# Performance work log

Hardware: AMD Instinct MI355X
Metric: run time of the kernel (lower is better)

Reference implementation:

```python
import jax, jax.numpy as jnp
import numpy as np

B, H, W = 8, 56, 56
DIM = 1792      # 256 + 512 + 1024 concatenated WRN50-2 feature channels
C_OUT = 1792    # dim // gamma_d with gamma_d = 1
M = 3136        # memory bank entries = scale**2 // gamma_c (gamma_c = 1)
K = 3           # num_nearest_neighbors


def setup_inputs() -> dict:
    key = jax.random.key(0)
    ks = jax.random.split(key, 6)
    f1 = jax.random.normal(ks[0], (B, 256, 56, 56), jnp.float32)
    f2 = jax.random.normal(ks[1], (B, 512, 28, 28), jnp.float32)
    f3 = jax.random.normal(ks[2], (B, 1024, 14, 14), jnp.float32)
    conv_w = jax.random.normal(ks[3], (C_OUT, DIM + 2), jnp.float32) / np.float32(np.sqrt(DIM + 2))
    conv_b = jax.random.normal(ks[4], (C_OUT,), jnp.float32) * 0.01
    memory_bank = jax.random.normal(ks[5], (C_OUT, M), jnp.float32)
    return {"f1": f1, "f2": f2, "f3": f3, "conv_w": conv_w, "conv_b": conv_b,
            "memory_bank": memory_bank}


def _avg_pool3(x):
    # F.avg_pool2d(x, 3, 1, 1), count_include_pad=True (torch default)
    s = jax.lax.reduce_window(x, 0.0, jax.lax.add, (1, 1, 3, 3), (1, 1, 1, 1),
                              ((0, 0), (0, 0), (1, 1), (1, 1)))
    return s / 9.0


def _descriptor(f1, f2, f3, conv_w, conv_b):
    o1 = _avg_pool3(f1)                                                    # [B,256,56,56]
    o2 = jax.image.resize(_avg_pool3(f2), (B, 512, H, W), method="bilinear")
    o3 = jax.image.resize(_avg_pool3(f3), (B, 1024, H, W), method="bilinear")
    sample = jnp.concatenate([o1, o2, o3], axis=1)                         # [B,DIM,H,W]
    # CoordConv: append x and y coordinate channels in [-1, 1]
    xx = jnp.tile(jnp.linspace(-1.0, 1.0, W, dtype=sample.dtype)[None, :], (H, 1))
    yy = jnp.tile(jnp.linspace(-1.0, 1.0, H, dtype=sample.dtype)[:, None], (1, W))
    coords = jnp.broadcast_to(jnp.stack([xx, yy])[None], (B, 2, H, W))
    inp = jnp.concatenate([sample, coords], axis=1)                        # [B,DIM+2,H,W]
    # 1x1 conv == per-pixel GEMM
    return jnp.einsum("bchw,oc->bohw", inp, conv_w) + conv_b[None, :, None, None]


def reference(f1, f2, f3, conv_w, conv_b, memory_bank):
    phi = _descriptor(f1, f2, f3, conv_w, conv_b)          # [B,C,H,W]
    feats = phi.reshape(B, C_OUT, H * W).transpose(0, 2, 1)  # [B,HW,C]
    # squared-distance expansion vs memory bank [C,M]
    f_sq = jnp.sum(feats * feats, axis=2, keepdims=True)     # [B,HW,1]
    c_sq = jnp.sum(memory_bank * memory_bank, axis=0, keepdims=True)  # [1,M]
    dist = f_sq + c_sq - 2.0 * jnp.einsum("bnc,cm->bnm", feats, memory_bank)  # [B,HW,M]
    dist = jnp.sqrt(dist)
    neg_top, _ = jax.lax.top_k(-dist, K)   # smallest K, ascending after negation
    d_k = -neg_top                         # [B,HW,K] sorted ascending
    w = jax.nn.softmax(-d_k, axis=-1)      # softmin
    score = w[:, :, 0] * d_k[:, :, 0]      # [B,HW]
    return score.reshape(B, 1, H, W)
```

## Files before the change

### kernel.cpp

```cpp
#include <hip/hip_runtime.h>
#include <hip/hip_bf16.h>
#include <math.h>

#define HH 56
#define WW 56
#define HWv 3136
#define NROWS 25088
#define DIMK 1792
#define KP   1920
#define CIN 1794
#define COUT 1792
#define MM 3136
#define MROWS 3328
#define JT2 13
#define JT1 7
#define NT 98

typedef __bf16 bf16_t;
typedef __bf16 bf16x8 __attribute__((ext_vector_type(8)));
typedef float f32x4 __attribute__((ext_vector_type(4)));

__device__ __forceinline__ void merge3(float& d0, float& d1, float& d2,
                                       float e0, float e1, float e2) {
    bool t0 = d0 <= e0;
    float c0 = t0 ? d0 : e0;
    float x0 = t0 ? d1 : d0, x1 = t0 ? d2 : d1;
    float y0 = t0 ? e0 : e1, y1 = t0 ? e1 : e2;
    bool t1 = x0 <= y0;
    float c1 = t1 ? x0 : y0;
    float c2 = t1 ? fminf(x1, y0) : fminf(x0, y1);
    d0 = c0; d1 = c1; d2 = c2;
}

__device__ __forceinline__ int xcd_swz(int wg, int nwg) {
    int x = wg & 7, idx = wg >> 3;
    int q = nwg >> 3, r = nwg & 7;
    return (x < r ? x * (q + 1) : r * (q + 1) + (x - r) * q) + idx;
}

__device__ __forceinline__ void block_bar() {
    asm volatile("" ::: "memory");
    __builtin_amdgcn_s_barrier();
    asm volatile("" ::: "memory");
}


__global__ __launch_bounds__(256) void k_convw(const float* __restrict__ cw, bf16_t* __restrict__ wb) {
    int idx = blockIdx.x * 256 + threadIdx.x;
    if (idx >= COUT * DIMK) return;
    int o = idx / DIMK, c = idx - o * DIMK;
    wb[(size_t)o * KP + c] = (bf16_t)cw[(size_t)o * CIN + c];
}

__global__ __launch_bounds__(256) void k_bankT(const float* __restrict__ bank, bf16_t* __restrict__ bt) {
    __shared__ float tile[64][65];
    int mt = blockIdx.x * 64;
    int ct = blockIdx.y * 64;
    int l = threadIdx.x & 63;
    int q = threadIdx.x >> 6;
    if (mt < MM) {
        #pragma unroll
        for (int r = 0; r < 16; ++r) {
            int cl = q * 16 + r;
            tile[cl][l] = bank[(size_t)(ct + cl) * MM + mt + l];
        }
        __syncthreads();
        #pragma unroll
        for (int r = 0; r < 16; ++r) {
            int ml = q * 16 + r;
            bt[(size_t)(mt + ml) * KP + ct + l] = (bf16_t)tile[l][ml];
        }
    } else {
        #pragma unroll
        for (int r = 0; r < 16; ++r) {
            int ml = q * 16 + r;
            bt[(size_t)(mt + ml) * KP + ct + l] = (bf16_t)0.f;
        }
    }
}

__global__ __launch_bounds__(256) void k_rowsq(const bf16_t* __restrict__ rows, float* __restrict__ sq) {
    int n = blockIdx.x * 4 + (threadIdx.x >> 6);
    int lane = threadIdx.x & 63;
    const bf16x8* row = (const bf16x8*)(rows + (size_t)n * KP);
    float s = 0.f;
    #pragma unroll
    for (int t = 0; t < 4; ++t) {
        int idx = t * 64 + lane;
        if (idx < 224) {
            bf16x8 v = row[idx];
            #pragma unroll
            for (int j = 0; j < 8; ++j) { float f = (float)v[j]; s += f * f; }
        }
    }
    #pragma unroll
    for (int off = 32; off; off >>= 1) s += __shfl_xor(s, off, 64);
    if (lane == 0) sq[n] = s;
}

__global__ __launch_bounds__(256) void k_pool_s(const float* __restrict__ in, float* __restrict__ out,
                                                int S, int total) {
    int idx = blockIdx.x * 256 + threadIdx.x;
    if (idx >= total) return;
    int x = idx % S; int y = (idx / S) % S; int bc = idx / (S * S);
    const float* base = in + (size_t)bc * S * S;
    float s = 0.f;
    for (int dy = -1; dy <= 1; ++dy) {
        int yy = y + dy; if ((unsigned)yy >= (unsigned)S) continue;
        for (int dx = -1; dx <= 1; ++dx) {
            int xx = x + dx; if ((unsigned)xx >= (unsigned)S) continue;
            s += base[yy * S + xx];
        }
    }
    out[idx] = s * (1.f / 9.f);
}

__global__ __launch_bounds__(256) void k_resize_p(const float* __restrict__ src, bf16_t* __restrict__ dst,
                                                  int S, int total, float scale, float shift) {
    int idx = blockIdx.x * 256 + threadIdx.x;
    if (idx >= total) return;
    int w = idx % WW; int h = (idx / WW) % HH; int bc = idx / HWv;
    float sy = scale * h + shift;
    float sx = scale * w + shift;
    float y0f = floorf(sy), x0f = floorf(sx);
    int y0 = (int)y0f, x0 = (int)x0f;
    float fy = sy - y0f, fx = sx - x0f;
    int iy0 = y0 < 0 ? 0 : (y0 > S - 1 ? S - 1 : y0);
    int iy1 = (y0 + 1) < 0 ? 0 : ((y0 + 1) > S - 1 ? S - 1 : y0 + 1);
    int ix0 = x0 < 0 ? 0 : (x0 > S - 1 ? S - 1 : x0);
    int ix1 = (x0 + 1) < 0 ? 0 : ((x0 + 1) > S - 1 ? S - 1 : x0 + 1);
    const float* base = src + (size_t)bc * S * S;
    float v00 = base[iy0 * S + ix0], v01 = base[iy0 * S + ix1];
    float v10 = base[iy1 * S + ix0], v11 = base[iy1 * S + ix1];
    float v = (1.f - fy) * ((1.f - fx) * v00 + fx * v01) + fy * ((1.f - fx) * v10 + fx * v11);
    dst[idx] = (bf16_t)v;
}

template <typename T>
__global__ __launch_bounds__(256) void k_transp(const T* __restrict__ src, bf16_t* __restrict__ inp,
                                                int Csrc, int coff) {
    __shared__ float tile[64][65];
    int hw0 = blockIdx.x * 64;
    int c0 = blockIdx.y * 64;
    int b = blockIdx.z;
    int l = threadIdx.x & 63;
    int q = threadIdx.x >> 6;
    #pragma unroll
    for (int r = 0; r < 16; ++r) {
        int c = q * 16 + r;
        tile[c][l] = (float)src[(size_t)(b * Csrc + c0 + c) * HWv + hw0 + l];
    }
    __syncthreads();
    #pragma unroll
    for (int r = 0; r < 16; ++r) {
        int ml = q * 16 + r;
        inp[(size_t)(b * HWv + hw0 + ml) * KP + coff + c0 + l] = (bf16_t)tile[l][ml];
    }
}


__device__ __forceinline__ void gemm256(const bf16_t* __restrict__ A, const bf16_t* __restrict__ Bm,
                                        int n0, int j0, f32x4 (&acc)[8][4], bf16_t* lds) {
    const int tid = threadIdx.x;
    const int lane = tid & 63;
    const int wid = tid >> 6;
    const int wr = wid >> 2;
    const int wc = wid & 3;
    const int lr = lane & 15;
    const int lg = lane >> 4;

    bf16_t* sA = lds;
    bf16_t* sB = lds + 32768;

    #pragma unroll
    for (int i = 0; i < 8; ++i)
        #pragma unroll
        for (int j = 0; j < 4; ++j) acc[i][j] = (f32x4){0.f, 0.f, 0.f, 0.f};

    auto stage = [&](bf16_t* dst, const bf16_t* src, int row0, int kc) {
        #pragma unroll
        for (int r = 0; r < 2; ++r) {
            int g = r * 512 + tid;
            int rp = g >> 2;
            int gc = g & 3;
            int gcs = gc ^ ((rp >> 1) & 3);
            __builtin_amdgcn_global_load_lds(
                (__attribute__((address_space(1))) void*)(src + (size_t)(row0 + rp) * KP + kc + gcs * 8),
                (__attribute__((address_space(3))) void*)(dst + g * 8), 16, 0, 0);
        }
    };

#define PHASE(BUF, MH, KH, STAGE_CODE, TAIL_CODE)                                          \
    {                                                                                      \
        bf16_t* au = sA + (BUF) * 16384 + (KH) * 8192;                                     \
        bf16_t* bu = sB + (BUF) * 16384 + (KH) * 8192;                                     \
        bf16x8 aF[4], bF[4];                                                               \
        _Pragma("unroll")                                                                  \
        for (int q = 0; q < 4; ++q) {                                                      \
            int ra = wr * 128 + (MH) * 64 + q * 16 + lr;                                   \
            aF[q] = *(const bf16x8*)(au + ra * 32 + ((lg ^ ((ra >> 1) & 3)) * 8));         \
            int rb = wc * 64 + q * 16 + lr;                                                \
            bF[q] = *(const bf16x8*)(bu + rb * 32 + ((lg ^ ((rb >> 1) & 3)) * 8));         \
        }                                                                                  \
        STAGE_CODE;                                                                        \
        block_bar();                                                                       \
        __builtin_amdgcn_s_setprio(1);                                                     \
        _Pragma("unroll")                                                                  \
        for (int q = 0; q < 4; ++q)                                                        \
            _Pragma("unroll")                                                              \
            for (int fn = 0; fn < 4; ++fn)                                                 \
                acc[(MH) * 4 + q][fn] = __builtin_amdgcn_mfma_f32_16x16x32_bf16(           \
                    aF[q], bF[fn], acc[(MH) * 4 + q][fn], 0, 0, 0);                        \
        __builtin_amdgcn_s_setprio(0);                                                     \
        TAIL_CODE;                                                                         \
        block_bar();                                                                       \
    }

    stage(sA + 0,             A,  n0, 0);
    stage(sB + 0,             Bm, j0, 0);
    stage(sA + 8192,          A,  n0, 32);
    stage(sB + 8192,          Bm, j0, 32);
    stage(sA + 16384,         A,  n0, 64);
    stage(sB + 16384,         Bm, j0, 64);
    asm volatile("s_waitcnt vmcnt(4)" ::: "memory");
    block_bar();

    for (int i = 0; i < 14; ++i) {
        int k1 = (2 * i + 1) * 64, k2 = (2 * i + 2) * 64, k3 = (2 * i + 3) * 64;
        PHASE(0, 0, 0, { stage(sA + 16384 + 8192, A,  n0, k1 + 32); }, {});
        PHASE(0, 1, 0, { stage(sB + 16384 + 8192, Bm, j0, k1 + 32); }, {});
        PHASE(0, 0, 1, { stage(sA + 0,            A,  n0, k2); }, {});
        PHASE(0, 1, 1, { stage(sB + 0,            Bm, j0, k2); },
              { asm volatile("s_waitcnt vmcnt(4)" ::: "memory"); });
        PHASE(1, 0, 0, { stage(sA + 8192,         A,  n0, k2 + 32); }, {});
        PHASE(1, 1, 0, { stage(sB + 8192,         Bm, j0, k2 + 32); }, {});
        PHASE(1, 0, 1, { stage(sA + 16384,        A,  n0, k3); }, {});
        PHASE(1, 1, 1, { stage(sB + 16384,        Bm, j0, k3); },
              { asm volatile("s_waitcnt vmcnt(4)" ::: "memory"); });
    }
    asm volatile("s_waitcnt vmcnt(0)" ::: "memory");
    block_bar();
#undef PHASE
}

__global__ __launch_bounds__(512) void k_gemm1(const bf16_t* __restrict__ inp, const bf16_t* __restrict__ wb,
                                               const float* __restrict__ cw, const float* __restrict__ cb,
                                               bf16_t* __restrict__ feats) {
    __shared__ __align__(16) bf16_t lds[65536];
    int wg = xcd_swz(blockIdx.x, NT * JT1);
    int n0 = (wg / JT1) * 256, j0 = (wg % JT1) * 256;
    f32x4 acc[8][4];
    gemm256(inp, wb, n0, j0, acc, lds);

    const int lane = threadIdx.x & 63, wid = threadIdx.x >> 6;
    const int wr = wid >> 2, wc = wid & 3, lr = lane & 15, lg = lane >> 4;
    float w1[4], w2[4], bb[4];
    int oc[4];
    #pragma unroll
    for (int fn = 0; fn < 4; ++fn) {
        int o = j0 + wc * 64 + fn * 16 + lr;
        oc[fn] = o;
        bb[fn] = cb[o];
        w1[fn] = cw[(size_t)o * CIN + DIMK];
        w2[fn] = cw[(size_t)o * CIN + DIMK + 1];
    }
    #pragma unroll
    for (int mh = 0; mh < 2; ++mh) {
        #pragma unroll
        for (int q = 0; q < 4; ++q) {
            #pragma unroll
            for (int v = 0; v < 4; ++v) {
                int n = n0 + wr * 128 + mh * 64 + q * 16 + lg * 4 + v;
                int hw = n % HWv;
                int h = hw / WW, w = hw - h * WW;
                float xx = (2.f / 55.f) * w - 1.f;
                float yy = (2.f / 55.f) * h - 1.f;
                #pragma unroll
                for (int fn = 0; fn < 4; ++fn) {
                    float phi = acc[mh * 4 + q][fn][v] + bb[fn] + xx * w1[fn] + yy * w2[fn];
                    feats[(size_t)n * KP + oc[fn]] = (bf16_t)phi;
                }
            }
        }
    }
}

__global__ __launch_bounds__(512) void k_gemm2(const bf16_t* __restrict__ feats, const bf16_t* __restrict__ bt,
                                               const float* __restrict__ csq, float* __restrict__ partial) {
    __shared__ __align__(16) bf16_t lds[65536];
    int wg = xcd_swz(blockIdx.x, NT * JT2);
    int nt = wg / JT2, jt = wg % JT2;
    int n0 = nt * 256, j0 = jt * 256;
    f32x4 acc[8][4];
    gemm256(feats, bt, n0, j0, acc, lds);

    const int tid = threadIdx.x;
    const int lane = tid & 63, wid = tid >> 6;
    const int wr = wid >> 2, wc = wid & 3, lr = lane & 15, lg = lane >> 4;

    float csqv[4];
    bool mval[4];
    #pragma unroll
    for (int fn = 0; fn < 4; ++fn) {
        int m = j0 + wc * 64 + fn * 16 + lr;
        mval[fn] = (m < MM);
        csqv[fn] = mval[fn] ? csq[m] : 0.f;
    }

    float* lf  = (float*)lds;
    float* lf2 = lf + 128 * 64 * 3;
    const int gidx = wc * 16 + lr;
    const float BIG = 3.0e38f;

    for (int pass = 0; pass < 2; ++pass) {
        if (wr == pass) {
            #pragma unroll
            for (int mh = 0; mh < 2; ++mh) {
                #pragma unroll
                for (int q = 0; q < 4; ++q) {
                    #pragma unroll
                    for (int v = 0; v < 4; ++v) {
                        float a0 = mval[0] ? csqv[0] - 2.f * acc[mh * 4 + q][0][v] : BIG;
                        float a1 = mval[1] ? csqv[1] - 2.f * acc[mh * 4 + q][1][v] : BIG;
                        float a2 = mval[2] ? csqv[2] - 2.f * acc[mh * 4 + q][2][v] : BIG;
                        float a3 = mval[3] ? csqv[3] - 2.f * acc[mh * 4 + q][3][v] : BIG;
                        float t;
                        if (a0 > a1) { t = a0; a0 = a1; a1 = t; }
                        if (a2 > a3) { t = a2; a2 = a3; a3 = t; }
                        if (a0 > a2) { t = a0; a0 = a2; a2 = t; }
                        if (a1 > a3) { t = a1; a1 = a3; a3 = t; }
                        if (a1 > a2) { t = a1; a1 = a2; a2 = t; }
                        int rl = mh * 64 + q * 16 + lg * 4 + v;
                        int bix = (rl * 64 + gidx) * 3;
                        lf[bix] = a0; lf[bix + 1] = a1; lf[bix + 2] = a2;
                    }
                }
            }
        }
        __syncthreads();
        {
            int row = tid >> 2, seg = tid & 3;
            int base = (row * 64 + seg * 16) * 3;
            float d0 = lf[base], d1 = lf[base + 1], d2 = lf[base + 2];
            #pragma unroll
            for (int j2 = 1; j2 < 16; ++j2)
                merge3(d0, d1, d2, lf[base + j2 * 3], lf[base + j2 * 3 + 1], lf[base + j2 * 3 + 2]);
            int o2 = (row * 4 + seg) * 3;
            lf2[o2] = d0; lf2[o2 + 1] = d1; lf2[o2 + 2] = d2;
        }
        __syncthreads();
        if (tid < 128) {
            int base = tid * 12;
            float d0 = lf2[base], d1 = lf2[base + 1], d2 = lf2[base + 2];
            #pragma unroll
            for (int sg = 1; sg < 4; ++sg)
                merge3(d0, d1, d2, lf2[base + sg * 3], lf2[base + sg * 3 + 1], lf2[base + sg * 3 + 2]);
            size_t grow = (size_t)(n0 + pass * 128 + tid);
            float* pp = partial + grow * (JT2 * 3) + jt * 3;
            pp[0] = d0; pp[1] = d1; pp[2] = d2;
        }
        __syncthreads();
    }
}

__global__ __launch_bounds__(256) void k_score(const float* __restrict__ partial, const float* __restrict__ fsq,
                                               float* __restrict__ out) {
    int row = blockIdx.x * 256 + threadIdx.x;
    if (row >= NROWS) return;
    const float* p = partial + (size_t)row * (JT2 * 3);
    float d0 = p[0], d1 = p[1], d2 = p[2];
    #pragma unroll
    for (int jt = 1; jt < JT2; ++jt)
        merge3(d0, d1, d2, p[jt * 3], p[jt * 3 + 1], p[jt * 3 + 2]);
    float fs = fsq[row];
    d0 = sqrtf(fmaxf(fs + d0, 0.f));
    d1 = sqrtf(fmaxf(fs + d1, 0.f));
    d2 = sqrtf(fmaxf(fs + d2, 0.f));
    float e1 = expf(d0 - d1), e2 = expf(d0 - d2);
    out[row] = d0 / (1.f + e1 + e2);
}


extern "C" void kernel_launch(void* const* d_in, const int* in_sizes, int n_in,
                              void* d_out, int out_size, void* d_ws, size_t ws_size,
                              hipStream_t stream) {
    const float* f1   = (const float*)d_in[0];
    const float* f2   = (const float*)d_in[1];
    const float* f3   = (const float*)d_in[2];
    const float* cw   = (const float*)d_in[3];
    const float* cb   = (const float*)d_in[4];
    const float* bank = (const float*)d_in[5];
    float* out = (float*)d_out;
    char* ws = (char*)d_ws;

    size_t off = 0;
    auto alloc = [&](size_t bytes) { size_t o = off; off = (off + bytes + 255) & ~(size_t)255; return o; };
    bf16_t* wb      = (bf16_t*)(ws + alloc((size_t)COUT * KP * 2));
    bf16_t* bt      = (bf16_t*)(ws + alloc((size_t)MROWS * KP * 2));
    float*  fsq     = (float*)(ws + alloc((size_t)NROWS * 4));
    float*  csq     = (float*)(ws + alloc((size_t)MM * 4));
    float*  partial = (float*)(ws + alloc((size_t)NROWS * JT2 * 3 * 4));
    bf16_t* inp     = (bf16_t*)(ws + alloc((size_t)NROWS * KP * 2));
    bf16_t* feats   = (bf16_t*)(ws + alloc((size_t)NROWS * KP * 2));

    char* fb = (char*)feats;
    float*  p1  = (float*)fb;
    float*  p2s = (float*)(fb + 25690112);
    bf16_t* r2b = (bf16_t*)(fb + 25690112 + 12845056);
    float*  p3s = (float*)fb;
    bf16_t* r3b = (bf16_t*)(fb + 6422528);

    k_convw<<<dim3((COUT * DIMK + 255) / 256), dim3(256), 0, stream>>>(cw, wb);
    k_bankT<<<dim3(MROWS / 64, DIMK / 64), dim3(256), 0, stream>>>(bank, bt);
    k_rowsq<<<dim3(MM / 4), dim3(256), 0, stream>>>(bt, csq);

    k_pool_s<<<dim3((8 * 256 * HWv + 255) / 256), dim3(256), 0, stream>>>(f1, p1, 56, 8 * 256 * HWv);
    k_pool_s<<<dim3((8 * 512 * 784 + 255) / 256), dim3(256), 0, stream>>>(f2, p2s, 28, 8 * 512 * 784);
    k_resize_p<<<dim3((8 * 512 * HWv + 255) / 256), dim3(256), 0, stream>>>(p2s, r2b, 28, 8 * 512 * HWv, 0.5f, -0.25f);
    k_transp<float><<<dim3(HWv / 64, 256 / 64, 8), dim3(256), 0, stream>>>(p1, inp, 256, 0);
    k_transp<bf16_t><<<dim3(HWv / 64, 512 / 64, 8), dim3(256), 0, stream>>>(r2b, inp, 512, 256);
    k_pool_s<<<dim3((8 * 1024 * 196 + 255) / 256), dim3(256), 0, stream>>>(f3, p3s, 14, 8 * 1024 * 196);
    k_resize_p<<<dim3((8 * 1024 * HWv + 255) / 256), dim3(256), 0, stream>>>(p3s, r3b, 14, 8 * 1024 * HWv, 0.25f, -0.375f);
    k_transp<bf16_t><<<dim3(HWv / 64, 1024 / 64, 8), dim3(256), 0, stream>>>(r3b, inp, 1024, 768);

    k_gemm1<<<dim3(NT * JT1), dim3(512), 0, stream>>>(inp, wb, cw, cb, feats);
    k_rowsq<<<dim3(NROWS / 4), dim3(256), 0, stream>>>(feats, fsq);
    k_gemm2<<<dim3(NT * JT2), dim3(512), 0, stream>>>(feats, bt, csq, partial);
    k_score<<<dim3((NROWS + 255) / 256), dim3(256), 0, stream>>>(partial, fsq, out);
}
```

Baseline: 753.1 us.

## Restructure GEMM mainloop into ring-buffered K-slices and use shuffle top-3 reduction

Replaces the double-buffered phase macro in the shared 256x256 GEMM with a rolling ring of 5 A slots and 4 B slots (K=32 each). Each iteration loads all 8x4 fragments, issues the next stage, and runs 32 MFMAs per barrier. Addresses and swizzle offsets are precomputed, and the LDS swizzle is reworked to pair rows. The gemm2 epilogue now does its top-3 merge with cross-lane shuffles instead of two-pass LDS staging, which cuts LDS traffic and barriers. The cost is more LDS per block (144KB) and higher register pressure from holding all fragments at once.

```diff
diff --git a/kernel.cpp b/kernel.cpp
--- a/kernel.cpp
+++ b/kernel.cpp
@@ -15,6 +15,7 @@
 #define JT2 13
 #define JT1 7
 #define NT 98
+#define NPH 56
 
 typedef __bf16 bf16_t;
 typedef __bf16 bf16x8 __attribute__((ext_vector_type(8)));
@@ -170,83 +171,107 @@
     const int lg = lane >> 4;
 
     bf16_t* sA = lds;
-    bf16_t* sB = lds + 32768;
-
-    #pragma unroll
-    for (int i = 0; i < 8; ++i)
-        #pragma unroll
-        for (int j = 0; j < 4; ++j) acc[i][j] = (f32x4){0.f, 0.f, 0.f, 0.f};
-
-    auto stage = [&](bf16_t* dst, const bf16_t* src, int row0, int kc) {
-        #pragma unroll
-        for (int r = 0; r < 2; ++r) {
-            int g = r * 512 + tid;
-            int rp = g >> 2;
-            int gc = g & 3;
-            int gcs = gc ^ ((rp >> 1) & 3);
+    bf16_t* sB = lds + 40960;
+
+    #pragma unroll
+    for (int m = 0; m < 8; ++m)
+        #pragma unroll
+        for (int n = 0; n < 4; ++n) acc[m][n] = (f32x4){0.f, 0.f, 0.f, 0.f};
+
+    size_t srcA[2], srcB[2];
+    int ldso[2];
+    #pragma unroll
+    for (int r = 0; r < 2; ++r) {
+        int g = r * 512 + tid;
+        int r2 = g >> 3, S = g & 7;
+        int G = S ^ (r2 & 7);
+        int row = 2 * r2 + (G >> 2);
+        int kgr = G & 3;
+        srcA[r] = (size_t)(n0 + row) * KP + kgr * 8;
+        srcB[r] = (size_t)(j0 + row) * KP + kgr * 8;
+        ldso[r] = g * 8;
+    }
+    auto stageA = [&](int slotOff, int kc) {
+        #pragma unroll
+        for (int r = 0; r < 2; ++r)
             __builtin_amdgcn_global_load_lds(
-                (__attribute__((address_space(1))) void*)(src + (size_t)(row0 + rp) * KP + kc + gcs * 8),
-                (__attribute__((address_space(3))) void*)(dst + g * 8), 16, 0, 0);
-        }
+                (__attribute__((address_space(1))) void*)(A + srcA[r] + kc),
+                (__attribute__((address_space(3))) void*)(sA + slotOff + ldso[r]), 16, 0, 0);
     };
-
-#define PHASE(BUF, MH, KH, STAGE_CODE, TAIL_CODE)                                          \
-    {                                                                                      \
-        bf16_t* au = sA + (BUF) * 16384 + (KH) * 8192;                                     \
-        bf16_t* bu = sB + (BUF) * 16384 + (KH) * 8192;                                     \
-        bf16x8 aF[4], bF[4];                                                               \
-        _Pragma("unroll")                                                                  \
-        for (int q = 0; q < 4; ++q) {                                                      \
-            int ra = wr * 128 + (MH) * 64 + q * 16 + lr;                                   \
-            aF[q] = *(const bf16x8*)(au + ra * 32 + ((lg ^ ((ra >> 1) & 3)) * 8));         \
-            int rb = wc * 64 + q * 16 + lr;                                                \
-            bF[q] = *(const bf16x8*)(bu + rb * 32 + ((lg ^ ((rb >> 1) & 3)) * 8));         \
-        }                                                                                  \
-        STAGE_CODE;                                                                        \
-        block_bar();                                                                       \
-        __builtin_amdgcn_s_setprio(1);                                                     \
-        _Pragma("unroll")                                                                  \
-        for (int q = 0; q < 4; ++q)                                                        \
-            _Pragma("unroll")                                                              \
-            for (int fn = 0; fn < 4; ++fn)                                                 \
-                acc[(MH) * 4 + q][fn] = __builtin_amdgcn_mfma_f32_16x16x32_bf16(           \
-                    aF[q], bF[fn], acc[(MH) * 4 + q][fn], 0, 0, 0);                        \
-        __builtin_amdgcn_s_setprio(0);                                                     \
-        TAIL_CODE;                                                                         \
-        block_bar();                                                                       \
-    }
-
-    stage(sA + 0,             A,  n0, 0);
-    stage(sB + 0,             Bm, j0, 0);
-    stage(sA + 8192,          A,  n0, 32);
-    stage(sB + 8192,          Bm, j0, 32);
-    stage(sA + 16384,         A,  n0, 64);
-    stage(sB + 16384,         Bm, j0, 64);
-    asm volatile("s_waitcnt vmcnt(4)" ::: "memory");
+    auto stageB = [&](int slotOff, int kc) {
+        #pragma unroll
+        for (int r = 0; r < 2; ++r)
+            __builtin_amdgcn_global_load_lds(
+                (__attribute__((address_space(1))) void*)(Bm + srcB[r] + kc),
+                (__attribute__((address_space(3))) void*)(sB + slotOff + ldso[r]), 16, 0, 0);
+    };
+
+    int offA[8], offB[4];
+    #pragma unroll
+    for (int m = 0; m < 8; ++m) {
+        int rowU = wr * 128 + m * 16 + lr;
+        int r2 = rowU >> 1, par = rowU & 1;
+        int G = par * 4 + lg;
+        offA[m] = r2 * 64 + (G ^ (r2 & 7)) * 8;
+    }
+    #pragma unroll
+    for (int n = 0; n < 4; ++n) {
+        int colU = wc * 64 + n * 16 + lr;
+        int r2 = colU >> 1, par = colU & 1;
+        int G = par * 4 + lg;
+        offB[n] = r2 * 64 + (G ^ (r2 & 7)) * 8;
+    }
+
+    stageA(0 * 8192, 0 * 32);
+    stageA(1 * 8192, 1 * 32);
+    stageB(0 * 8192, 0 * 32);
+    stageA(2 * 8192, 2 * 32);
+    stageB(1 * 8192, 1 * 32);
+    stageA(3 * 8192, 3 * 32);
+    stageB(2 * 8192, 2 * 32);
+    asm volatile("s_waitcnt vmcnt(8)" ::: "memory");
     block_bar();
 
-    for (int i = 0; i < 14; ++i) {
-        int k1 = (2 * i + 1) * 64, k2 = (2 * i + 2) * 64, k3 = (2 * i + 3) * 64;
-        PHASE(0, 0, 0, { stage(sA + 16384 + 8192, A,  n0, k1 + 32); }, {});
-        PHASE(0, 1, 0, { stage(sB + 16384 + 8192, Bm, j0, k1 + 32); }, {});
-        PHASE(0, 0, 1, { stage(sA + 0,            A,  n0, k2); }, {});
-        PHASE(0, 1, 1, { stage(sB + 0,            Bm, j0, k2); },
-              { asm volatile("s_waitcnt vmcnt(4)" ::: "memory"); });
-        PHASE(1, 0, 0, { stage(sA + 8192,         A,  n0, k2 + 32); }, {});
-        PHASE(1, 1, 0, { stage(sB + 8192,         Bm, j0, k2 + 32); }, {});
-        PHASE(1, 0, 1, { stage(sA + 16384,        A,  n0, k3); }, {});
-        PHASE(1, 1, 1, { stage(sB + 16384,        Bm, j0, k3); },
-              { asm volatile("s_waitcnt vmcnt(4)" ::: "memory"); });
+    int roA = 0, roB = 0;
+    int kcA = 4 * 32, kcB = 3 * 32;
+
+    for (int p = 0; p < NPH; ++p) {
+        bf16x8 aF[8], bF[4];
+        #pragma unroll
+        for (int m = 0; m < 8; ++m)
+            aF[m] = *(const bf16x8*)(sA + roA + offA[m]);
+        #pragma unroll
+        for (int n = 0; n < 4; ++n)
+            bF[n] = *(const bf16x8*)(sB + roB + offB[n]);
+
+        int stA = roA - 8192; if (stA < 0) stA = 4 * 8192;
+        int stB = roB - 8192; if (stB < 0) stB = 3 * 8192;
+        stageA(stA, kcA);
+        stageB(stB, kcB);
+        kcA += 32; kcB += 32;
+
+        __builtin_amdgcn_s_setprio(1);
+        #pragma unroll
+        for (int m = 0; m < 8; ++m)
+            #pragma unroll
+            for (int n = 0; n < 4; ++n)
+                acc[m][n] = __builtin_amdgcn_mfma_f32_16x16x32_bf16(
+                    aF[m], bF[n], acc[m][n], 0, 0, 0);
+        __builtin_amdgcn_s_setprio(0);
+
+        roA += 8192; if (roA == 5 * 8192) roA = 0;
+        roB += 8192; if (roB == 4 * 8192) roB = 0;
+        asm volatile("s_waitcnt vmcnt(8)" ::: "memory");
+        block_bar();
     }
     asm volatile("s_waitcnt vmcnt(0)" ::: "memory");
-    block_bar();
-#undef PHASE
-}
+}
+
 
 __global__ __launch_bounds__(512) void k_gemm1(const bf16_t* __restrict__ inp, const bf16_t* __restrict__ wb,
                                                const float* __restrict__ cw, const float* __restrict__ cb,
                                                bf16_t* __restrict__ feats) {
-    __shared__ __align__(16) bf16_t lds[65536];
+    __shared__ __align__(16) bf16_t lds[73728];
     int wg = xcd_swz(blockIdx.x, NT * JT1);
     int n0 = (wg / JT1) * 256, j0 = (wg % JT1) * 256;
     f32x4 acc[8][4];
@@ -257,29 +282,26 @@
     float w1[4], w2[4], bb[4];
     int oc[4];
     #pragma unroll
-    for (int fn = 0; fn < 4; ++fn) {
-        int o = j0 + wc * 64 + fn * 16 + lr;
-        oc[fn] = o;
-        bb[fn] = cb[o];
-        w1[fn] = cw[(size_t)o * CIN + DIMK];
-        w2[fn] = cw[(size_t)o * CIN + DIMK + 1];
-    }
-    #pragma unroll
-    for (int mh = 0; mh < 2; ++mh) {
-        #pragma unroll
-        for (int q = 0; q < 4; ++q) {
+    for (int n = 0; n < 4; ++n) {
+        int o = j0 + wc * 64 + n * 16 + lr;
+        oc[n] = o;
+        bb[n] = cb[o];
+        w1[n] = cw[(size_t)o * CIN + DIMK];
+        w2[n] = cw[(size_t)o * CIN + DIMK + 1];
+    }
+    #pragma unroll
+    for (int m = 0; m < 8; ++m) {
+        #pragma unroll
+        for (int v = 0; v < 4; ++v) {
+            int nrow = n0 + wr * 128 + m * 16 + lg * 4 + v;
+            int hw = nrow % HWv;
+            int h = hw / WW, w = hw - h * WW;
+            float xx = (2.f / 55.f) * w - 1.f;
+            float yy = (2.f / 55.f) * h - 1.f;
             #pragma unroll
-            for (int v = 0; v < 4; ++v) {
-                int n = n0 + wr * 128 + mh * 64 + q * 16 + lg * 4 + v;
-                int hw = n % HWv;
-                int h = hw / WW, w = hw - h * WW;
-                float xx = (2.f / 55.f) * w - 1.f;
-                float yy = (2.f / 55.f) * h - 1.f;
-                #pragma unroll
-                for (int fn = 0; fn < 4; ++fn) {
-                    float phi = acc[mh * 4 + q][fn][v] + bb[fn] + xx * w1[fn] + yy * w2[fn];
-                    feats[(size_t)n * KP + oc[fn]] = (bf16_t)phi;
-                }
+            for (int n = 0; n < 4; ++n) {
+                float phi = acc[m][n][v] + bb[n] + xx * w1[n] + yy * w2[n];
+                feats[(size_t)nrow * KP + oc[n]] = (bf16_t)phi;
             }
         }
     }
@@ -287,79 +309,69 @@
 
 __global__ __launch_bounds__(512) void k_gemm2(const bf16_t* __restrict__ feats, const bf16_t* __restrict__ bt,
                                                const float* __restrict__ csq, float* __restrict__ partial) {
-    __shared__ __align__(16) bf16_t lds[65536];
+    __shared__ __align__(16) bf16_t lds[73728];
     int wg = xcd_swz(blockIdx.x, NT * JT2);
     int nt = wg / JT2, jt = wg % JT2;
     int n0 = nt * 256, j0 = jt * 256;
     f32x4 acc[8][4];
     gemm256(feats, bt, n0, j0, acc, lds);
 
+    block_bar();
+
     const int tid = threadIdx.x;
     const int lane = tid & 63, wid = tid >> 6;
     const int wr = wid >> 2, wc = wid & 3, lr = lane & 15, lg = lane >> 4;
+    const float BIG = 3.0e38f;
 
     float csqv[4];
     bool mval[4];
     #pragma unroll
-    for (int fn = 0; fn < 4; ++fn) {
-        int m = j0 + wc * 64 + fn * 16 + lr;
-        mval[fn] = (m < MM);
-        csqv[fn] = mval[fn] ? csq[m] : 0.f;
-    }
-
-    float* lf  = (float*)lds;
-    float* lf2 = lf + 128 * 64 * 3;
-    const int gidx = wc * 16 + lr;
-    const float BIG = 3.0e38f;
-
-    for (int pass = 0; pass < 2; ++pass) {
-        if (wr == pass) {
+    for (int n = 0; n < 4; ++n) {
+        int m = j0 + wc * 64 + n * 16 + lr;
+        mval[n] = (m < MM);
+        csqv[n] = mval[n] ? csq[m] : 0.f;
+    }
+
+    float* lf = (float*)lds;
+
+    #pragma unroll
+    for (int m = 0; m < 8; ++m) {
+        #pragma unroll
+        for (int v = 0; v < 4; ++v) {
+            float a0 = mval[0] ? csqv[0] - 2.f * acc[m][0][v] : BIG;
+            float a1 = mval[1] ? csqv[1] - 2.f * acc[m][1][v] : BIG;
+            float a2 = mval[2] ? csqv[2] - 2.f * acc[m][2][v] : BIG;
+            float a3 = mval[3] ? csqv[3] - 2.f * acc[m][3][v] : BIG;
+            float t;
+            if (a0 > a1) { t = a0; a0 = a1; a1 = t; }
+            if (a2 > a3) { t = a2; a2 = a3; a3 = t; }
+            if (a0 > a2) { t = a0; a0 = a2; a2 = t; }
+            if (a1 > a3) { t = a1; a1 = a3; a3 = t; }
+            if (a1 > a2) { t = a1; a1 = a2; a2 = t; }
+            float d0 = a0, d1 = a1, d2 = a2;
             #pragma unroll
-            for (int mh = 0; mh < 2; ++mh) {
-                #pragma unroll
-                for (int q = 0; q < 4; ++q) {
-                    #pragma unroll
-                    for (int v = 0; v < 4; ++v) {
-                        float a0 = mval[0] ? csqv[0] - 2.f * acc[mh * 4 + q][0][v] : BIG;
-                        float a1 = mval[1] ? csqv[1] - 2.f * acc[mh * 4 + q][1][v] : BIG;
-                        float a2 = mval[2] ? csqv[2] - 2.f * acc[mh * 4 + q][2][v] : BIG;
-                        float a3 = mval[3] ? csqv[3] - 2.f * acc[mh * 4 + q][3][v] : BIG;
-                        float t;
-                        if (a0 > a1) { t = a0; a0 = a1; a1 = t; }
-                        if (a2 > a3) { t = a2; a2 = a3; a3 = t; }
-                        if (a0 > a2) { t = a0; a0 = a2; a2 = t; }
-                        if (a1 > a3) { t = a1; a1 = a3; a3 = t; }
-                        if (a1 > a2) { t = a1; a1 = a2; a2 = t; }
-                        int rl = mh * 64 + q * 16 + lg * 4 + v;
-                        int bix = (rl * 64 + gidx) * 3;
-                        lf[bix] = a0; lf[bix + 1] = a1; lf[bix + 2] = a2;
-                    }
-                }
+            for (int off = 1; off < 16; off <<= 1) {
+                float e0 = __shfl_xor(d0, off, 64);
+                float e1 = __shfl_xor(d1, off, 64);
+                float e2 = __shfl_xor(d2, off, 64);
+                merge3(d0, d1, d2, e0, e1, e2);
             }
-        }
-        __syncthreads();
-        {
-            int row = tid >> 2, seg = tid & 3;
-            int base = (row * 64 + seg * 16) * 3;
-            float d0 = lf[base], d1 = lf[base + 1], d2 = lf[base + 2];
-            #pragma unroll
-            for (int j2 = 1; j2 < 16; ++j2)
-                merge3(d0, d1, d2, lf[base + j2 * 3], lf[base + j2 * 3 + 1], lf[base + j2 * 3 + 2]);
-            int o2 = (row * 4 + seg) * 3;
-            lf2[o2] = d0; lf2[o2 + 1] = d1; lf2[o2 + 2] = d2;
-        }
-        __syncthreads();
-        if (tid < 128) {
-            int base = tid * 12;
-            float d0 = lf2[base], d1 = lf2[base + 1], d2 = lf2[base + 2];
-            #pragma unroll
-            for (int sg = 1; sg < 4; ++sg)
-                merge3(d0, d1, d2, lf2[base + sg * 3], lf2[base + sg * 3 + 1], lf2[base + sg * 3 + 2]);
-            size_t grow = (size_t)(n0 + pass * 128 + tid);
-            float* pp = partial + grow * (JT2 * 3) + jt * 3;
-            pp[0] = d0; pp[1] = d1; pp[2] = d2;
-        }
-        __syncthreads();
+            if (lr == 0) {
+                int rowl = wr * 128 + m * 16 + lg * 4 + v;
+                int bix = (rowl * 4 + wc) * 3;
+                lf[bix] = d0; lf[bix + 1] = d1; lf[bix + 2] = d2;
+            }
+        }
+    }
+    __syncthreads();
+    if (tid < 256) {
+        int base = tid * 12;
+        float d0 = lf[base], d1 = lf[base + 1], d2 = lf[base + 2];
+        #pragma unroll
+        for (int q = 1; q < 4; ++q)
+            merge3(d0, d1, d2, lf[base + q * 3], lf[base + q * 3 + 1], lf[base + q * 3 + 2]);
+        float* pp = partial + (size_t)(n0 + tid) * (JT2 * 3) + jt * 3;
+        pp[0] = d0; pp[1] = d1; pp[2] = d2;
     }
 }
 
```

Result: slower. 784.9 us (+4.2%).
